# Optimization experiments

Hardware: AMD Instinct MI355X
Metric: run time of the kernel (lower is better)

Reference implementation:

```python
import jax, jax.numpy as jnp
import numpy as np

N = 50000      # nodes
E = 800000     # edges (before self-loops)
F_IN = 768     # num_features
H = 128        # hidden_dim
C = 9          # num_classes
M = 3          # num_mid_layers
BN_EPS = 1e-5

def _glorot(k, shape):
    lim = float(np.sqrt(6.0 / (shape[-2] + shape[-1])))
    return jax.random.uniform(k, shape, jnp.float32, -lim, lim)

def setup_inputs() -> dict:
    key = jax.random.key(0)
    ks = jax.random.split(key, 24)
    x = jax.random.normal(ks[0], (N, F_IN), jnp.float32)
    edge_index = jax.random.randint(ks[1], (2, E), 0, N)
    edge_type = jax.random.randint(ks[2], (E,), 0, 5)
    edge_distance = jax.random.uniform(ks[3], (E,), jnp.float32)
    # GATConv params (heads=1): W [in,out], att_src/att_dst [out], bias [out]
    W0 = _glorot(ks[4], (F_IN, H)); a0s = _glorot(ks[5], (1, H))[0]; a0d = _glorot(ks[6], (1, H))[0]; b0 = jnp.zeros((H,), jnp.float32)
    Wm = _glorot(ks[7], (M, H, H)); ams = _glorot(ks[8], (M, 1, H))[:, 0]; amd = _glorot(ks[9], (M, 1, H))[:, 0]; bm = jnp.zeros((M, H), jnp.float32)
    W4 = _glorot(ks[10], (H, C)); a4s = _glorot(ks[11], (1, C))[0]; a4d = _glorot(ks[12], (1, C))[0]; b4 = jnp.zeros((C,), jnp.float32)
    # BatchNorm params for the M+1 norms actually used in forward (all dim H)
    gamma = jnp.ones((M + 1, H), jnp.float32)
    beta = jnp.zeros((M + 1, H), jnp.float32)
    return {"x": x, "edge_index": edge_index, "edge_type": edge_type, "edge_distance": edge_distance,
            "W0": W0, "a0s": a0s, "a0d": a0d, "b0": b0,
            "Wm": Wm, "ams": ams, "amd": amd, "bm": bm,
            "W4": W4, "a4s": a4s, "a4d": a4d, "b4": b4,
            "gamma": gamma, "beta": beta}

def _leaky(x, s):
    return jnp.where(x >= 0, x, s * x)

def _gat_conv(x, src, dst, W, a_s, a_d, b):
    # x: [N, in] -> h: [N, out]; attention per edge j->i, softmax over incoming edges of i
    h = x @ W
    alpha_src = h @ a_s            # [N]
    alpha_dst = h @ a_d            # [N]
    e = _leaky(alpha_src[src] + alpha_dst[dst], 0.2)   # [Etot]
    m = jax.ops.segment_max(e, dst, num_segments=N)
    ex = jnp.exp(e - m[dst])
    z = jax.ops.segment_sum(ex, dst, num_segments=N)
    alpha = ex / z[dst]
    out = jax.ops.segment_sum(h[src] * alpha[:, None], dst, num_segments=N)
    return out + b

def _bn_train(x, g, be):
    mu = x.mean(0)
    var = x.var(0)   # biased, as BatchNorm1d uses for normalization
    return (x - mu) * jax.lax.rsqrt(var + BN_EPS) * g + be

def reference(x, edge_index, edge_type, edge_distance,
              W0, a0s, a0d, b0, Wm, ams, amd, bm, W4, a4s, a4d, b4, gamma, beta):
    loops = jnp.arange(N, dtype=edge_index.dtype)
    src = jnp.concatenate([edge_index[0], loops])   # add self-loops (PyG default)
    dst = jnp.concatenate([edge_index[1], loops])
    h = _gat_conv(x, src, dst, W0, a0s, a0d, b0)
    for i in range(M):
        t = _leaky(_bn_train(h, gamma[i], beta[i]), 0.1)
        h = _gat_conv(t, src, dst, Wm[i], ams[i], amd[i], bm[i]) + t
    h = _leaky(_bn_train(h, gamma[M], beta[M]), 0.1)
    h = _gat_conv(h, src, dst, W4, a4s, a4d, b4)
    return _leaky(h, 0.1)
```

## Files before the change

### kernel.cpp

```cpp
#include <hip/hip_runtime.h>
#include <hip/hip_bf16.h>

#define N_NODES 50000
#define N_EDGES 800000
#define F_INN   768
#define HID     128
#define N_CLS   9
#define ETOT    (N_EDGES + N_NODES)
#define BN_EPS  1e-5f

typedef __hip_bfloat16 bf16;
typedef __attribute__((ext_vector_type(8))) short bf16x8;
typedef __attribute__((ext_vector_type(4))) float f32x4;

__device__ __forceinline__ float leaky(float v, float s) { return v >= 0.0f ? v : s * v; }
__device__ __forceinline__ int clampn(int s) {
  return ((unsigned)s < (unsigned)N_NODES) ? s : 0;
}
__device__ __forceinline__ short f2bs(float f) {
  bf16 h = __float2bfloat16(f);
  return __builtin_bit_cast(short, h);
}
__device__ __forceinline__ float bs2f(unsigned short u) {
  unsigned v = ((unsigned)u) << 16;
  return __builtin_bit_cast(float, v);
}
__device__ __forceinline__ void gload_lds16(const void* g, void* l) {
  __builtin_amdgcn_global_load_lds((const __attribute__((address_space(1))) void*)g,
                                   (__attribute__((address_space(3))) void*)l, 16, 0, 0);
}

__global__ void k_pack(const float* __restrict__ W0, const float* __restrict__ Wm,
                       short* __restrict__ W0T, short* __restrict__ WmT) {
  int i = blockIdx.x * blockDim.x + threadIdx.x;
  if (i < F_INN * HID) {
    int n = i / F_INN, k = i % F_INN;
    W0T[i] = f2bs(W0[k * HID + n]);
  } else if (i < F_INN * HID + 3 * HID * HID) {
    int j = i - F_INN * HID;
    int l = j / (HID * HID), rem = j % (HID * HID);
    int n = rem / HID, k = rem % HID;
    WmT[j] = f2bs(Wm[(l * HID + k) * HID + n]);
  }
}

__global__ void k_zero(float* p, int n) {
  int i = blockIdx.x * blockDim.x + threadIdx.x;
  if (i < n) p[i] = 0.0f;
}

__global__ void k_init_deg(int* fill) {
  int i = blockIdx.x * blockDim.x + threadIdx.x;
  if (i < N_NODES) fill[i] = 1;
}

__global__ void k_count(const int* __restrict__ dst, int* fill) {
  int e = blockIdx.x * blockDim.x + threadIdx.x;
  if (e < N_EDGES) atomicAdd(&fill[clampn(dst[e])], 1);
}

__global__ void k_scan(int* fill, int* row_ptr) {
  __shared__ int wsum[16], wpre[16];
  int tid = threadIdx.x, lane = tid & 63, wv = tid >> 6;
  int carry = 0;
  for (int base = 0; base < N_NODES; base += 1024) {
    int i = base + tid;
    int v = (i < N_NODES) ? fill[i] : 0;
    if (i < N_NODES) fill[i] = 0;
    int sc = v;
#pragma unroll
    for (int off = 1; off < 64; off <<= 1) {
      int t = __shfl_up(sc, off);
      if (lane >= off) sc += t;
    }
    if (lane == 63) wsum[wv] = sc;
    __syncthreads();
    if (tid < 16) {
      int s = wsum[tid];
#pragma unroll
      for (int off = 1; off < 16; off <<= 1) {
        int t = __shfl_up(s, off);
        if (tid >= off) s += t;
      }
      wpre[tid] = s;
    }
    __syncthreads();
    int woff = wv ? wpre[wv - 1] : 0;
    if (i < N_NODES) row_ptr[i] = carry + woff + sc - v;
    carry += wpre[15];
    __syncthreads();
  }
  if (tid == 0) row_ptr[N_NODES] = carry;
}

__global__ void k_place(const int* __restrict__ src, const int* __restrict__ dst,
                        const int* __restrict__ row_ptr, int* fill, int* csr_src) {
  int id = blockIdx.x * blockDim.x + threadIdx.x;
  if (id >= ETOT) return;
  int s, d;
  if (id < N_EDGES) { s = clampn(src[id]); d = clampn(dst[id]); }
  else { s = id - N_EDGES; d = s; }
  int p = atomicAdd(&fill[d], 1);
  csr_src[row_ptr[d] + p] = s;
}

template <int K, bool BN>
__global__ __launch_bounds__(256, 2)
void k_gemm_mfma(const float* __restrict__ X, const short* __restrict__ BT,
                 const float* __restrict__ scale, const float* __restrict__ shift,
                 const float* __restrict__ a_s, const float* __restrict__ a_d,
                 short* __restrict__ hb, float* __restrict__ asrc,
                 float* __restrict__ adst) {
  constexpr int NP = K / 64;
  constexpr int NB = 4;
  __shared__ short sB[NB][8192];
  int tid = threadIdx.x;
  int w = tid >> 6, lane = tid & 63;
  int m = lane & 15, q = lane >> 4;
  int row0 = blockIdx.x * 64 + w * 16;
  int rowm = row0 + m;
  int rowc = (rowm < N_NODES) ? rowm : 0;
  const float* xbase = X + (size_t)rowc * K + q * 8;
  const short* gb = BT + (size_t)m * K + q * 8;

  f32x4 acc[8];
#pragma unroll
  for (int t = 0; t < 8; ++t) acc[t] = (f32x4){0.f, 0.f, 0.f, 0.f};
  float4 xr[NB][4];

  float scf[K / 32][8], sff[K / 32][8];
  if (BN) {
#pragma unroll
    for (int c = 0; c < K / 32; ++c) {
      int kb = c * 32 + q * 8;
      *(float4*)(&scf[c][0]) = *(const float4*)(scale + kb);
      *(float4*)(&scf[c][4]) = *(const float4*)(scale + kb + 4);
      *(float4*)(&sff[c][0]) = *(const float4*)(shift + kb);
      *(float4*)(&sff[c][4]) = *(const float4*)(shift + kb + 4);
    }
  }

  auto issue = [&](int p) {
    const int buf = p & (NB - 1);
#pragma unroll
    for (int c = 0; c < 4; ++c) {
      int ci = w * 4 + c;
      int t = ci >> 1, kk = ci & 1;
      gload_lds16(gb + (size_t)t * 16 * K + p * 64 + kk * 32, &sB[buf][ci * 512]);
    }
    xr[buf][0] = *(const float4*)(xbase + p * 64);
    xr[buf][1] = *(const float4*)(xbase + p * 64 + 4);
    xr[buf][2] = *(const float4*)(xbase + p * 64 + 32);
    xr[buf][3] = *(const float4*)(xbase + p * 64 + 36);
  };

  issue(0);
  if (NP > 1) issue(1);

#pragma unroll
  for (int p = 0; p < NP; ++p) {
    if (p + 2 < NP) issue(p + 2);
    if (p + 2 < NP)      asm volatile("s_waitcnt vmcnt(16)" ::: "memory");
    else if (p + 1 < NP) asm volatile("s_waitcnt vmcnt(8)" ::: "memory");
    else                 asm volatile("s_waitcnt vmcnt(0)" ::: "memory");
    __builtin_amdgcn_s_barrier();

    const int cur = p & (NB - 1);
    const char* sbb = (const char*)&sB[cur][0] + ((size_t)lane << 4);
#pragma unroll
    for (int kk = 0; kk < 2; ++kk) {
      float xv[8];
      *(float4*)(xv)     = xr[cur][kk * 2];
      *(float4*)(xv + 4) = xr[cur][kk * 2 + 1];
      if (BN) {
#pragma unroll
        for (int j = 0; j < 8; ++j)
          xv[j] = leaky(xv[j] * scf[p * 2 + kk][j] + sff[p * 2 + kk][j], 0.1f);
      }
      bf16x8 a;
#pragma unroll
      for (int j = 0; j < 8; ++j) a[j] = f2bs(xv[j]);
#pragma unroll
      for (int t = 0; t < 8; ++t) {
        bf16x8 b = *(const bf16x8*)(sbb + ((t * 2 + kk) << 10));
        acc[t] = __builtin_amdgcn_mfma_f32_16x16x32_bf16(a, b, acc[t], 0, 0, 0);
      }
    }
  }

  float sr[4] = {0.f, 0.f, 0.f, 0.f}, dr[4] = {0.f, 0.f, 0.f, 0.f};
  int rowq = row0 + q * 4;
#pragma unroll
  for (int t = 0; t < 8; ++t) {
    float av = a_s[t * 16 + m], dv = a_d[t * 16 + m];
#pragma unroll
    for (int r = 0; r < 4; ++r) {
      float c = acc[t][r];
      if (rowq + r < N_NODES)
        hb[(size_t)(rowq + r) * HID + t * 16 + m] = f2bs(c);
      sr[r] += c * av;
      dr[r] += c * dv;
    }
  }
#pragma unroll
  for (int r = 0; r < 4; ++r) {
#pragma unroll
    for (int off = 1; off < 16; off <<= 1) {
      sr[r] += __shfl_xor(sr[r], off);
      dr[r] += __shfl_xor(dr[r], off);
    }
  }
  if (m == 0) {
#pragma unroll
    for (int r = 0; r < 4; ++r) {
      if (rowq + r < N_NODES) {
        asrc[rowq + r] = sr[r];
        adst[rowq + r] = dr[r];
      }
    }
  }
}

__device__ __forceinline__ void acc8(float* a, float e, uint4 v) {
  a[0] += e * bs2f((unsigned short)(v.x & 0xffffu));
  a[1] += e * bs2f((unsigned short)(v.x >> 16));
  a[2] += e * bs2f((unsigned short)(v.y & 0xffffu));
  a[3] += e * bs2f((unsigned short)(v.y >> 16));
  a[4] += e * bs2f((unsigned short)(v.z & 0xffffu));
  a[5] += e * bs2f((unsigned short)(v.z >> 16));
  a[6] += e * bs2f((unsigned short)(v.w & 0xffffu));
  a[7] += e * bs2f((unsigned short)(v.w >> 16));
}

__global__ void k_agg128(const unsigned short* __restrict__ h, const float* __restrict__ asrc,
                         const float* __restrict__ adst, const int* __restrict__ row_ptr,
                         const int* __restrict__ csr_src, const float* __restrict__ bias,
                         const float* __restrict__ hres, const float* __restrict__ scale,
                         const float* __restrict__ shift, float* __restrict__ out) {
  __shared__ int   lds_ss[4][64];
  __shared__ float lds_ex[4][64];
  int wid = (blockIdx.x * blockDim.x + threadIdx.x) >> 6;
  int lane = threadIdx.x & 63;
  int w = (threadIdx.x >> 6) & 3;
  if (wid >= N_NODES) return;
  int beg = row_ptr[wid], end = row_ptr[wid + 1];
  float adsti = adst[wid];
  float mx = -1e30f;
  for (int cb = beg; cb < end; cb += 64) {
    int e = cb + lane;
    if (e < end) {
      int s = clampn(csr_src[e]);
      mx = fmaxf(mx, leaky(asrc[s] + adsti, 0.2f));
    }
  }
#pragma unroll
  for (int off = 1; off < 64; off <<= 1) mx = fmaxf(mx, __shfl_xor(mx, off));
  int g = lane & 15;
  int es = lane >> 4;
  float z = 0.f;
  float a[8];
#pragma unroll
  for (int k = 0; k < 8; ++k) a[k] = 0.f;
  for (int cb = beg; cb < end; cb += 64) {
    int cnt = min(64, end - cb);
    int sl = 0;
    float ex = 0.f;
    if (lane < cnt) {
      sl = clampn(csr_src[cb + lane]);
      ex = __expf(leaky(asrc[sl] + adsti, 0.2f) - mx);
    }
    lds_ss[w][lane] = sl;
    lds_ex[w][lane] = ex;
    __builtin_amdgcn_wave_barrier();
    float zp = ex;
#pragma unroll
    for (int off = 1; off < 64; off <<= 1) zp += __shfl_xor(zp, off);
    z += zp;
    for (int jb = 0; jb < cnt; jb += 8) {
      int j0 = jb + es, j1 = jb + 4 + es;
      int s0 = lds_ss[w][j0]; float e0 = lds_ex[w][j0];
      int s1 = lds_ss[w][j1]; float e1 = lds_ex[w][j1];
      uint4 v0 = *(const uint4*)(h + (size_t)s0 * HID + g * 8);
      uint4 v1 = *(const uint4*)(h + (size_t)s1 * HID + g * 8);
      acc8(a, e0, v0);
      acc8(a, e1, v1);
    }
    __builtin_amdgcn_wave_barrier();
  }
#pragma unroll
  for (int k = 0; k < 8; ++k) {
    a[k] += __shfl_xor(a[k], 16);
    a[k] += __shfl_xor(a[k], 32);
  }
  float inv = (z > 0.0f) ? 1.0f / z : 0.0f;
  if (lane < 16) {
    int c0 = g * 8;
    float hr[8];
    if (scale) {
      *(float4*)(hr)     = *(const float4*)(hres + (size_t)wid * HID + c0);
      *(float4*)(hr + 4) = *(const float4*)(hres + (size_t)wid * HID + c0 + 4);
    }
    float o[8];
#pragma unroll
    for (int k = 0; k < 8; ++k) {
      o[k] = a[k] * inv + bias[c0 + k];
      if (scale) o[k] += leaky(hr[k] * scale[c0 + k] + shift[c0 + k], 0.1f);
    }
    *(float4*)(out + (size_t)wid * HID + c0)     = *(float4*)(o);
    *(float4*)(out + (size_t)wid * HID + c0 + 4) = *(float4*)(o + 4);
  }
}

__global__ void k_bn_stats(const float* __restrict__ h, float* bnsum, float* bnsumsq) {
  int f = threadIdx.x;
  int r0 = blockIdx.x * 128;
  int r1 = min(r0 + 128, N_NODES);
  float s = 0.0f, s2 = 0.0f;
#pragma unroll 8
  for (int r = r0; r < r1; ++r) {
    float v = h[(size_t)r * HID + f];
    s += v;
    s2 += v * v;
  }
  atomicAdd(&bnsum[f], s);
  atomicAdd(&bnsumsq[f], s2);
}

__global__ void k_bn_final(const float* __restrict__ bnsum, const float* __restrict__ bnsumsq,
                           const float* __restrict__ gamma, const float* __restrict__ beta,
                           float* bnscale, float* bnshift) {
  int f = threadIdx.x;
  float mu = bnsum[f] / (float)N_NODES;
  float var = bnsumsq[f] / (float)N_NODES - mu * mu;
  var = fmaxf(var, 0.0f);
  float rstd = rsqrtf(var + BN_EPS);
  float g = gamma[f];
  bnscale[f] = g * rstd;
  bnshift[f] = beta[f] - mu * g * rstd;
}

__global__ void k_final_gemm(const float* __restrict__ h, const float* __restrict__ scale,
                             const float* __restrict__ shift, const float* __restrict__ W4,
                             const float* __restrict__ a4s, const float* __restrict__ a4d,
                             float* __restrict__ h4, float* __restrict__ asrc,
                             float* __restrict__ adst) {
  int row = (blockIdx.x * blockDim.x + threadIdx.x) >> 6;
  int lane = threadIdx.x & 63;
  if (row >= N_NODES) return;
  float t0 = leaky(h[(size_t)row * HID + lane] * scale[lane] + shift[lane], 0.1f);
  float t1 = leaky(h[(size_t)row * HID + 64 + lane] * scale[64 + lane] + shift[64 + lane], 0.1f);
  float myv = 0.0f, s = 0.0f, d = 0.0f;
#pragma unroll
  for (int c = 0; c < N_CLS; ++c) {
    float p = t0 * W4[lane * N_CLS + c] + t1 * W4[(lane + 64) * N_CLS + c];
#pragma unroll
    for (int m = 32; m; m >>= 1) p += __shfl_xor(p, m);
    s += p * a4s[c];
    d += p * a4d[c];
    if (lane == c) myv = p;
  }
  if (lane < N_CLS) h4[(size_t)row * N_CLS + lane] = myv;
  if (lane == 0) { asrc[row] = s; adst[row] = d; }
}

__global__ void k_final_agg(const float* __restrict__ h4, const float* __restrict__ asrc,
                            const float* __restrict__ adst, const int* __restrict__ row_ptr,
                            const int* __restrict__ csr_src, const float* __restrict__ b4,
                            float* __restrict__ out) {
  int wid = (blockIdx.x * blockDim.x + threadIdx.x) >> 6;
  int lane = threadIdx.x & 63;
  if (wid >= N_NODES) return;
  int beg = row_ptr[wid], end = row_ptr[wid + 1];
  float adsti = adst[wid];
  float mx = -1e30f;
  int e = beg;
  for (; e + 4 <= end; e += 4) {
    int s0 = clampn(csr_src[e]),     s1 = clampn(csr_src[e + 1]);
    int s2 = clampn(csr_src[e + 2]), s3 = clampn(csr_src[e + 3]);
    float v0 = leaky(asrc[s0] + adsti, 0.2f);
    float v1 = leaky(asrc[s1] + adsti, 0.2f);
    float v2 = leaky(asrc[s2] + adsti, 0.2f);
    float v3 = leaky(asrc[s3] + adsti, 0.2f);
    mx = fmaxf(mx, fmaxf(fmaxf(v0, v1), fmaxf(v2, v3)));
  }
  for (; e < end; ++e) {
    int s = clampn(csr_src[e]);
    mx = fmaxf(mx, leaky(asrc[s] + adsti, 0.2f));
  }
  float z = 0.0f, a = 0.0f;
  e = beg;
  for (; e + 4 <= end; e += 4) {
    int s0 = clampn(csr_src[e]),     s1 = clampn(csr_src[e + 1]);
    int s2 = clampn(csr_src[e + 2]), s3 = clampn(csr_src[e + 3]);
    float ex0 = __expf(leaky(asrc[s0] + adsti, 0.2f) - mx);
    float ex1 = __expf(leaky(asrc[s1] + adsti, 0.2f) - mx);
    float ex2 = __expf(leaky(asrc[s2] + adsti, 0.2f) - mx);
    float ex3 = __expf(leaky(asrc[s3] + adsti, 0.2f) - mx);
    z += (ex0 + ex1) + (ex2 + ex3);
    if (lane < N_CLS) {
      float h0 = h4[(size_t)s0 * N_CLS + lane];
      float h1 = h4[(size_t)s1 * N_CLS + lane];
      float h2 = h4[(size_t)s2 * N_CLS + lane];
      float h3 = h4[(size_t)s3 * N_CLS + lane];
      a += ex0 * h0 + ex1 * h1 + ex2 * h2 + ex3 * h3;
    }
  }
  for (; e < end; ++e) {
    int s = clampn(csr_src[e]);
    float ex = __expf(leaky(asrc[s] + adsti, 0.2f) - mx);
    z += ex;
    if (lane < N_CLS) a += ex * h4[(size_t)s * N_CLS + lane];
  }
  if (lane < N_CLS) {
    float o = (z > 0.0f) ? a / z : 0.0f;
    o = leaky(o + b4[lane], 0.1f);
    out[(size_t)wid * N_CLS + lane] = o;
  }
}

extern "C" void kernel_launch(void* const* d_in, const int* in_sizes, int n_in,
                              void* d_out, int out_size, void* d_ws, size_t ws_size,
                              hipStream_t stream) {
  const float* x   = (const float*)d_in[0];
  const int*   ei  = (const int*)d_in[1];
  const int*   src = ei;
  const int*   dst = ei + N_EDGES;
  const float* W0  = (const float*)d_in[4];
  const float* a0s = (const float*)d_in[5];
  const float* a0d = (const float*)d_in[6];
  const float* b0  = (const float*)d_in[7];
  const float* Wm  = (const float*)d_in[8];
  const float* ams = (const float*)d_in[9];
  const float* amd = (const float*)d_in[10];
  const float* bm  = (const float*)d_in[11];
  const float* W4  = (const float*)d_in[12];
  const float* a4s = (const float*)d_in[13];
  const float* a4d = (const float*)d_in[14];
  const float* b4  = (const float*)d_in[15];
  const float* gam = (const float*)d_in[16];
  const float* bet = (const float*)d_in[17];
  float* out = (float*)d_out;

  int* row_ptr   = (int*)d_ws;
  int* fill      = row_ptr + 50004;
  int* csr_src   = fill + N_NODES;
  short* W0T     = (short*)(csr_src + ETOT);
  short* WmT     = W0T + F_INN * HID;
  short* bufA    = WmT + 3 * HID * HID;
  float* asrc    = (float*)(bufA + (size_t)N_NODES * HID);
  float* adst    = asrc + N_NODES;
  float* bnsum   = adst + N_NODES;
  float* bnsumsq = bnsum + HID;
  float* bnscale = bnsumsq + HID;
  float* bnshift = bnscale + HID;
  float* h4      = bnshift + HID;
  float* bufB    = h4 + (size_t)N_NODES * N_CLS;

  const int B256 = 256;
  int gN    = (N_NODES + B256 - 1) / B256;
  int gE    = (N_EDGES + B256 - 1) / B256;
  int gET   = (ETOT + B256 - 1) / B256;
  int gWav  = (N_NODES + 3) / 4;
  int gMfma = (N_NODES + 63) / 64;
  int gBN   = (N_NODES + 127) / 128;
  int gPack = (F_INN * HID + 3 * HID * HID + B256 - 1) / B256;

  k_pack<<<gPack, B256, 0, stream>>>(W0, Wm, W0T, WmT);
  k_init_deg<<<gN, B256, 0, stream>>>(fill);
  k_count<<<gE, B256, 0, stream>>>(dst, fill);
  k_scan<<<1, 1024, 0, stream>>>(fill, row_ptr);
  k_place<<<gET, B256, 0, stream>>>(src, dst, row_ptr, fill, csr_src);

  k_gemm_mfma<F_INN, false><<<gMfma, B256, 0, stream>>>(x, W0T, nullptr, nullptr,
                                                        a0s, a0d, bufA, asrc, adst);
  k_agg128<<<gWav, B256, 0, stream>>>((const unsigned short*)bufA, asrc, adst, row_ptr,
                                      csr_src, b0, nullptr, nullptr, nullptr, bufB);

  for (int i = 0; i < 3; ++i) {
    k_zero<<<1, 256, 0, stream>>>(bnsum, 2 * HID);
    k_bn_stats<<<gBN, HID, 0, stream>>>(bufB, bnsum, bnsumsq);
    k_bn_final<<<1, HID, 0, stream>>>(bnsum, bnsumsq, gam + i * HID, bet + i * HID,
                                      bnscale, bnshift);
    k_gemm_mfma<HID, true><<<gMfma, B256, 0, stream>>>(bufB, WmT + i * HID * HID,
                                                       bnscale, bnshift,
                                                       ams + i * HID, amd + i * HID,
                                                       bufA, asrc, adst);
    k_agg128<<<gWav, B256, 0, stream>>>((const unsigned short*)bufA, asrc, adst, row_ptr,
                                        csr_src, bm + i * HID, bufB, bnscale, bnshift, bufB);
  }

  k_zero<<<1, 256, 0, stream>>>(bnsum, 2 * HID);
  k_bn_stats<<<gBN, HID, 0, stream>>>(bufB, bnsum, bnsumsq);
  k_bn_final<<<1, HID, 0, stream>>>(bnsum, bnsumsq, gam + 3 * HID, bet + 3 * HID,
                                    bnscale, bnshift);
  k_final_gemm<<<gWav, B256, 0, stream>>>(bufB, bnscale, bnshift, W4, a4s, a4d,
                                          h4, asrc, adst);
  k_final_agg<<<gWav, B256, 0, stream>>>(h4, asrc, adst, row_ptr, csr_src, b4, out);
}
```

Baseline: 950.9 us.

## Restructure GEMM tiling, fold BN finalize into consumers, add single-pass aggregation

The MFMA GEMM now handles 16 rows per 512-thread block. Each wave computes a 16-column slice, the X tile is staged in LDS with an XOR swizzle, and weights are register double-buffered from global. The separate zero and BN-finalize kernels are removed: consumers recompute scale and shift from the raw sums, and the aggregation kernel zeroes the next stats buffer through ping-pong buffers. Both aggregation kernels gain a single-pass path for nodes with at most 64 incoming edges, and the final aggregation is parallelised across edges within a wave. The risks are redundant per-thread BN math and more global weight traffic per block.

New measurement: 808.0 us. -15.0%, faster.

```diff
diff --git a/kernel.cpp b/kernel.cpp
--- a/kernel.cpp
+++ b/kernel.cpp
@@ -8,6 +8,7 @@
 #define N_CLS   9
 #define ETOT    (N_EDGES + N_NODES)
 #define BN_EPS  1e-5f
+#define INV_N   (1.0f / (float)N_NODES)
 
 typedef __hip_bfloat16 bf16;
 typedef __attribute__((ext_vector_type(8))) short bf16x8;
@@ -44,11 +45,6 @@
   }
 }
 
-__global__ void k_zero(float* p, int n) {
-  int i = blockIdx.x * blockDim.x + threadIdx.x;
-  if (i < n) p[i] = 0.0f;
-}
-
 __global__ void k_init_deg(int* fill) {
   int i = blockIdx.x * blockDim.x + threadIdx.x;
   if (i < N_NODES) fill[i] = 1;
@@ -105,102 +101,101 @@
 }
 
 template <int K, bool BN>
-__global__ __launch_bounds__(256, 2)
+__global__ __launch_bounds__(512, 5)
 void k_gemm_mfma(const float* __restrict__ X, const short* __restrict__ BT,
-                 const float* __restrict__ scale, const float* __restrict__ shift,
+                 const float* __restrict__ stats, const float* __restrict__ gamma,
+                 const float* __restrict__ beta,
                  const float* __restrict__ a_s, const float* __restrict__ a_d,
                  short* __restrict__ hb, float* __restrict__ asrc,
                  float* __restrict__ adst) {
-  constexpr int NP = K / 64;
-  constexpr int NB = 4;
-  __shared__ short sB[NB][8192];
+  constexpr int NS = K / 32;
+  constexpr int SPC = 4;
+  constexpr int CH = NS / SPC;
+  constexpr int ROWB = K * 4;
+  constexpr int XB = 16 * ROWB;
+  __shared__ float4 xs4[XB / 16];
+  __shared__ float psA[8][16], psD[8][16];
+  __shared__ float scs[HID], sfs[HID];
+  char* xs = (char*)xs4;
+
   int tid = threadIdx.x;
-  int w = tid >> 6, lane = tid & 63;
+  int wid = tid >> 6, lane = tid & 63;
   int m = lane & 15, q = lane >> 4;
-  int row0 = blockIdx.x * 64 + w * 16;
-  int rowm = row0 + m;
-  int rowc = (rowm < N_NODES) ? rowm : 0;
-  const float* xbase = X + (size_t)rowc * K + q * 8;
-  const short* gb = BT + (size_t)m * K + q * 8;
-
-  f32x4 acc[8];
-#pragma unroll
-  for (int t = 0; t < 8; ++t) acc[t] = (f32x4){0.f, 0.f, 0.f, 0.f};
-  float4 xr[NB][4];
-
-  float scf[K / 32][8], sff[K / 32][8];
-  if (BN) {
-#pragma unroll
-    for (int c = 0; c < K / 32; ++c) {
-      int kb = c * 32 + q * 8;
-      *(float4*)(&scf[c][0]) = *(const float4*)(scale + kb);
-      *(float4*)(&scf[c][4]) = *(const float4*)(scale + kb + 4);
-      *(float4*)(&sff[c][0]) = *(const float4*)(shift + kb);
-      *(float4*)(&sff[c][4]) = *(const float4*)(shift + kb + 4);
-    }
-  }
-
-  auto issue = [&](int p) {
-    const int buf = p & (NB - 1);
-#pragma unroll
-    for (int c = 0; c < 4; ++c) {
-      int ci = w * 4 + c;
-      int t = ci >> 1, kk = ci & 1;
-      gload_lds16(gb + (size_t)t * 16 * K + p * 64 + kk * 32, &sB[buf][ci * 512]);
-    }
-    xr[buf][0] = *(const float4*)(xbase + p * 64);
-    xr[buf][1] = *(const float4*)(xbase + p * 64 + 4);
-    xr[buf][2] = *(const float4*)(xbase + p * 64 + 32);
-    xr[buf][3] = *(const float4*)(xbase + p * 64 + 36);
+  int row0 = blockIdx.x * 16;
+  int col0 = wid * 16;
+
+  const short* bbase = BT + (size_t)(col0 + m) * K + q * 8;
+  f32x4 acc = (f32x4){0.f, 0.f, 0.f, 0.f};
+  bf16x8 bb0[SPC], bb1[SPC];
+
+  auto loadC = [&](bf16x8* dst, int c) {
+#pragma unroll
+    for (int i = 0; i < SPC; ++i)
+      dst[i] = *(const bf16x8*)(bbase + (size_t)(c * SPC + i) * 32);
   };
-
-  issue(0);
-  if (NP > 1) issue(1);
-
-#pragma unroll
-  for (int p = 0; p < NP; ++p) {
-    if (p + 2 < NP) issue(p + 2);
-    if (p + 2 < NP)      asm volatile("s_waitcnt vmcnt(16)" ::: "memory");
-    else if (p + 1 < NP) asm volatile("s_waitcnt vmcnt(8)" ::: "memory");
-    else                 asm volatile("s_waitcnt vmcnt(0)" ::: "memory");
-    __builtin_amdgcn_s_barrier();
-
-    const int cur = p & (NB - 1);
-    const char* sbb = (const char*)&sB[cur][0] + ((size_t)lane << 4);
-#pragma unroll
-    for (int kk = 0; kk < 2; ++kk) {
-      float xv[8];
-      *(float4*)(xv)     = xr[cur][kk * 2];
-      *(float4*)(xv + 4) = xr[cur][kk * 2 + 1];
+  auto computeC = [&](const bf16x8* bw, int c) {
+#pragma unroll
+    for (int i = 0; i < SPC; ++i) {
+      int s = c * SPC + i;
+      int kb = s * 128 + q * 32;
+      int sw = (m & 7) << 4;
+      float4 x0 = *(const float4*)(xs + m * ROWB + (kb ^ sw));
+      float4 x1 = *(const float4*)(xs + m * ROWB + ((kb + 16) ^ sw));
+      float xv[8] = {x0.x, x0.y, x0.z, x0.w, x1.x, x1.y, x1.z, x1.w};
       if (BN) {
-#pragma unroll
-        for (int j = 0; j < 8; ++j)
-          xv[j] = leaky(xv[j] * scf[p * 2 + kk][j] + sff[p * 2 + kk][j], 0.1f);
+        int k0 = s * 32 + q * 8;
+#pragma unroll
+        for (int j = 0; j < 8; ++j) xv[j] = leaky(xv[j] * scs[k0 + j] + sfs[k0 + j], 0.1f);
       }
       bf16x8 a;
 #pragma unroll
       for (int j = 0; j < 8; ++j) a[j] = f2bs(xv[j]);
-#pragma unroll
-      for (int t = 0; t < 8; ++t) {
-        bf16x8 b = *(const bf16x8*)(sbb + ((t * 2 + kk) << 10));
-        acc[t] = __builtin_amdgcn_mfma_f32_16x16x32_bf16(a, b, acc[t], 0, 0, 0);
-      }
-    }
-  }
-
-  float sr[4] = {0.f, 0.f, 0.f, 0.f}, dr[4] = {0.f, 0.f, 0.f, 0.f};
-  int rowq = row0 + q * 4;
-#pragma unroll
-  for (int t = 0; t < 8; ++t) {
-    float av = a_s[t * 16 + m], dv = a_d[t * 16 + m];
-#pragma unroll
-    for (int r = 0; r < 4; ++r) {
-      float c = acc[t][r];
-      if (rowq + r < N_NODES)
-        hb[(size_t)(rowq + r) * HID + t * 16 + m] = f2bs(c);
-      sr[r] += c * av;
-      dr[r] += c * dv;
-    }
+      acc = __builtin_amdgcn_mfma_f32_16x16x32_bf16(a, bw[i], acc, 0, 0, 0);
+    }
+  };
+
+  if (BN && tid < HID) {
+    float mu = stats[tid] * INV_N;
+    float var = fmaxf(stats[HID + tid] * INV_N - mu * mu, 0.0f);
+    float rs = rsqrtf(var + BN_EPS);
+    float g = gamma[tid];
+    scs[tid] = g * rs;
+    sfs[tid] = beta[tid] - mu * g * rs;
+  }
+
+  loadC(bb0, 0);
+  if (CH > 1) loadC(bb1, 1);
+  asm volatile("" ::: "memory");
+  constexpr int ROUNDS = XB / 8192;
+#pragma unroll
+  for (int r = 0; r < ROUNDS; ++r) {
+    int o = r * 8192 + tid * 16;
+    int row = o / ROWB;
+    int bb = o - row * ROWB;
+    int sw = (row & 7) << 4;
+    gload_lds16((const char*)X + (size_t)(row0 + row) * ROWB + (bb ^ sw), xs + o);
+  }
+  __syncthreads();
+
+#pragma unroll
+  for (int c = 0; c < CH; ++c) {
+    if (c & 1) {
+      computeC(bb1, c);
+      if (c + 2 < CH) { loadC(bb1, c + 2); asm volatile("" ::: "memory"); }
+    } else {
+      computeC(bb0, c);
+      if (c + 2 < CH) { loadC(bb0, c + 2); asm volatile("" ::: "memory"); }
+    }
+  }
+
+  float av = a_s[col0 + m], dv = a_d[col0 + m];
+  float sr[4], dr[4];
+#pragma unroll
+  for (int r = 0; r < 4; ++r) {
+    float cc = acc[r];
+    hb[(size_t)(row0 + q * 4 + r) * HID + col0 + m] = f2bs(cc);
+    sr[r] = cc * av;
+    dr[r] = cc * dv;
   }
 #pragma unroll
   for (int r = 0; r < 4; ++r) {
@@ -213,11 +208,17 @@
   if (m == 0) {
 #pragma unroll
     for (int r = 0; r < 4; ++r) {
-      if (rowq + r < N_NODES) {
-        asrc[rowq + r] = sr[r];
-        adst[rowq + r] = dr[r];
-      }
-    }
+      psA[wid][q * 4 + r] = sr[r];
+      psD[wid][q * 4 + r] = dr[r];
+    }
+  }
+  __syncthreads();
+  if (tid < 16) {
+    float s = 0.f, d = 0.f;
+#pragma unroll
+    for (int w2 = 0; w2 < 8; ++w2) { s += psA[w2][tid]; d += psD[w2][tid]; }
+    asrc[row0 + tid] = s;
+    adst[row0 + tid] = d;
   }
 }
 
@@ -235,83 +236,122 @@
 __global__ void k_agg128(const unsigned short* __restrict__ h, const float* __restrict__ asrc,
                          const float* __restrict__ adst, const int* __restrict__ row_ptr,
                          const int* __restrict__ csr_src, const float* __restrict__ bias,
-                         const float* __restrict__ hres, const float* __restrict__ scale,
-                         const float* __restrict__ shift, float* __restrict__ out) {
+                         const float* __restrict__ hres, const float* __restrict__ stats,
+                         const float* __restrict__ gamma, const float* __restrict__ beta,
+                         float* __restrict__ out, float* __restrict__ zeroP) {
   __shared__ int   lds_ss[4][64];
   __shared__ float lds_ex[4][64];
+  if (zeroP && blockIdx.x == 0 && threadIdx.x < 256) zeroP[threadIdx.x] = 0.0f;
   int wid = (blockIdx.x * blockDim.x + threadIdx.x) >> 6;
   int lane = threadIdx.x & 63;
   int w = (threadIdx.x >> 6) & 3;
   if (wid >= N_NODES) return;
   int beg = row_ptr[wid], end = row_ptr[wid + 1];
+  int cnt0 = end - beg;
   float adsti = adst[wid];
-  float mx = -1e30f;
-  for (int cb = beg; cb < end; cb += 64) {
-    int e = cb + lane;
-    if (e < end) {
-      int s = clampn(csr_src[e]);
-      mx = fmaxf(mx, leaky(asrc[s] + adsti, 0.2f));
-    }
-  }
-#pragma unroll
-  for (int off = 1; off < 64; off <<= 1) mx = fmaxf(mx, __shfl_xor(mx, off));
-  int g = lane & 15;
-  int es = lane >> 4;
+  int g = lane & 15, es = lane >> 4;
   float z = 0.f;
   float a[8];
 #pragma unroll
   for (int k = 0; k < 8; ++k) a[k] = 0.f;
-  for (int cb = beg; cb < end; cb += 64) {
-    int cnt = min(64, end - cb);
+
+  if (cnt0 <= 64) {
     int sl = 0;
-    float ex = 0.f;
-    if (lane < cnt) {
-      sl = clampn(csr_src[cb + lane]);
-      ex = __expf(leaky(asrc[sl] + adsti, 0.2f) - mx);
-    }
+    float v = -1e30f;
+    if (lane < cnt0) {
+      sl = clampn(csr_src[beg + lane]);
+      v = leaky(asrc[sl] + adsti, 0.2f);
+    }
+    float mx = v;
+#pragma unroll
+    for (int off = 1; off < 64; off <<= 1) mx = fmaxf(mx, __shfl_xor(mx, off));
+    float ex = (lane < cnt0) ? __expf(v - mx) : 0.f;
     lds_ss[w][lane] = sl;
     lds_ex[w][lane] = ex;
     __builtin_amdgcn_wave_barrier();
-    float zp = ex;
-#pragma unroll
-    for (int off = 1; off < 64; off <<= 1) zp += __shfl_xor(zp, off);
-    z += zp;
-    for (int jb = 0; jb < cnt; jb += 8) {
+    float zs = 0.f;
+    for (int jb = 0; jb < cnt0; jb += 8) {
       int j0 = jb + es, j1 = jb + 4 + es;
       int s0 = lds_ss[w][j0]; float e0 = lds_ex[w][j0];
       int s1 = lds_ss[w][j1]; float e1 = lds_ex[w][j1];
       uint4 v0 = *(const uint4*)(h + (size_t)s0 * HID + g * 8);
       uint4 v1 = *(const uint4*)(h + (size_t)s1 * HID + g * 8);
+      zs += e0 + e1;
       acc8(a, e0, v0);
       acc8(a, e1, v1);
     }
-    __builtin_amdgcn_wave_barrier();
+    z = zs;
+  } else {
+    float mx = -1e30f;
+    for (int cb = beg; cb < end; cb += 64) {
+      int e = cb + lane;
+      if (e < end) {
+        int s = clampn(csr_src[e]);
+        mx = fmaxf(mx, leaky(asrc[s] + adsti, 0.2f));
+      }
+    }
+#pragma unroll
+    for (int off = 1; off < 64; off <<= 1) mx = fmaxf(mx, __shfl_xor(mx, off));
+    float zs = 0.f;
+    for (int cb = beg; cb < end; cb += 64) {
+      int cnt = min(64, end - cb);
+      int sl = 0;
+      float ex = 0.f;
+      if (lane < cnt) {
+        sl = clampn(csr_src[cb + lane]);
+        ex = __expf(leaky(asrc[sl] + adsti, 0.2f) - mx);
+      }
+      lds_ss[w][lane] = sl;
+      lds_ex[w][lane] = ex;
+      __builtin_amdgcn_wave_barrier();
+      for (int jb = 0; jb < cnt; jb += 8) {
+        int j0 = jb + es, j1 = jb + 4 + es;
+        int s0 = lds_ss[w][j0]; float e0 = lds_ex[w][j0];
+        int s1 = lds_ss[w][j1]; float e1 = lds_ex[w][j1];
+        uint4 v0 = *(const uint4*)(h + (size_t)s0 * HID + g * 8);
+        uint4 v1 = *(const uint4*)(h + (size_t)s1 * HID + g * 8);
+        zs += e0 + e1;
+        acc8(a, e0, v0);
+        acc8(a, e1, v1);
+      }
+      __builtin_amdgcn_wave_barrier();
+    }
+    z = zs;
   }
 #pragma unroll
   for (int k = 0; k < 8; ++k) {
     a[k] += __shfl_xor(a[k], 16);
     a[k] += __shfl_xor(a[k], 32);
   }
+  z += __shfl_xor(z, 16);
+  z += __shfl_xor(z, 32);
   float inv = (z > 0.0f) ? 1.0f / z : 0.0f;
   if (lane < 16) {
     int c0 = g * 8;
-    float hr[8];
-    if (scale) {
+    float o[8];
+#pragma unroll
+    for (int k = 0; k < 8; ++k) o[k] = a[k] * inv + bias[c0 + k];
+    if (hres) {
+      float hr[8];
       *(float4*)(hr)     = *(const float4*)(hres + (size_t)wid * HID + c0);
       *(float4*)(hr + 4) = *(const float4*)(hres + (size_t)wid * HID + c0 + 4);
-    }
-    float o[8];
-#pragma unroll
-    for (int k = 0; k < 8; ++k) {
-      o[k] = a[k] * inv + bias[c0 + k];
-      if (scale) o[k] += leaky(hr[k] * scale[c0 + k] + shift[c0 + k], 0.1f);
+#pragma unroll
+      for (int k = 0; k < 8; ++k) {
+        int c = c0 + k;
+        float mu = stats[c] * INV_N;
+        float var = fmaxf(stats[HID + c] * INV_N - mu * mu, 0.0f);
+        float rs = rsqrtf(var + BN_EPS);
+        float sc = gamma[c] * rs;
+        float sf = beta[c] - mu * sc;
+        o[k] += leaky(hr[k] * sc + sf, 0.1f);
+      }
     }
     *(float4*)(out + (size_t)wid * HID + c0)     = *(float4*)(o);
     *(float4*)(out + (size_t)wid * HID + c0 + 4) = *(float4*)(o + 4);
   }
 }
 
-__global__ void k_bn_stats(const float* __restrict__ h, float* bnsum, float* bnsumsq) {
+__global__ void k_bn_stats(const float* __restrict__ h, float* stats) {
   int f = threadIdx.x;
   int r0 = blockIdx.x * 128;
   int r1 = min(r0 + 128, N_NODES);
@@ -322,33 +362,30 @@
     s += v;
     s2 += v * v;
   }
-  atomicAdd(&bnsum[f], s);
-  atomicAdd(&bnsumsq[f], s2);
-}
-
-__global__ void k_bn_final(const float* __restrict__ bnsum, const float* __restrict__ bnsumsq,
-                           const float* __restrict__ gamma, const float* __restrict__ beta,
-                           float* bnscale, float* bnshift) {
-  int f = threadIdx.x;
-  float mu = bnsum[f] / (float)N_NODES;
-  float var = bnsumsq[f] / (float)N_NODES - mu * mu;
-  var = fmaxf(var, 0.0f);
-  float rstd = rsqrtf(var + BN_EPS);
-  float g = gamma[f];
-  bnscale[f] = g * rstd;
-  bnshift[f] = beta[f] - mu * g * rstd;
-}
-
-__global__ void k_final_gemm(const float* __restrict__ h, const float* __restrict__ scale,
-                             const float* __restrict__ shift, const float* __restrict__ W4,
+  atomicAdd(&stats[f], s);
+  atomicAdd(&stats[HID + f], s2);
+}
+
+__global__ void k_final_gemm(const float* __restrict__ h, const float* __restrict__ stats,
+                             const float* __restrict__ gamma, const float* __restrict__ beta,
+                             const float* __restrict__ W4,
                              const float* __restrict__ a4s, const float* __restrict__ a4d,
                              float* __restrict__ h4, float* __restrict__ asrc,
                              float* __restrict__ adst) {
   int row = (blockIdx.x * blockDim.x + threadIdx.x) >> 6;
   int lane = threadIdx.x & 63;
   if (row >= N_NODES) return;
-  float t0 = leaky(h[(size_t)row * HID + lane] * scale[lane] + shift[lane], 0.1f);
-  float t1 = leaky(h[(size_t)row * HID + 64 + lane] * scale[64 + lane] + shift[64 + lane], 0.1f);
+  int c1 = lane + 64;
+  float mu0 = stats[lane] * INV_N;
+  float va0 = fmaxf(stats[HID + lane] * INV_N - mu0 * mu0, 0.0f);
+  float rs0 = rsqrtf(va0 + BN_EPS);
+  float sc0 = gamma[lane] * rs0, sf0 = beta[lane] - mu0 * sc0;
+  float mu1 = stats[c1] * INV_N;
+  float va1 = fmaxf(stats[HID + c1] * INV_N - mu1 * mu1, 0.0f);
+  float rs1 = rsqrtf(va1 + BN_EPS);
+  float sc1 = gamma[c1] * rs1, sf1 = beta[c1] - mu1 * sc1;
+  float t0 = leaky(h[(size_t)row * HID + lane] * sc0 + sf0, 0.1f);
+  float t1 = leaky(h[(size_t)row * HID + c1] * sc1 + sf1, 0.1f);
   float myv = 0.0f, s = 0.0f, d = 0.0f;
 #pragma unroll
   for (int c = 0; c < N_CLS; ++c) {
@@ -367,52 +404,75 @@
                             const float* __restrict__ adst, const int* __restrict__ row_ptr,
                             const int* __restrict__ csr_src, const float* __restrict__ b4,
                             float* __restrict__ out) {
+  __shared__ int   lds_ss[4][64];
+  __shared__ float lds_ex[4][64];
   int wid = (blockIdx.x * blockDim.x + threadIdx.x) >> 6;
   int lane = threadIdx.x & 63;
+  int w = (threadIdx.x >> 6) & 3;
   if (wid >= N_NODES) return;
   int beg = row_ptr[wid], end = row_ptr[wid + 1];
+  int cnt0 = end - beg;
   float adsti = adst[wid];
-  float mx = -1e30f;
-  int e = beg;
-  for (; e + 4 <= end; e += 4) {
-    int s0 = clampn(csr_src[e]),     s1 = clampn(csr_src[e + 1]);
-    int s2 = clampn(csr_src[e + 2]), s3 = clampn(csr_src[e + 3]);
-    float v0 = leaky(asrc[s0] + adsti, 0.2f);
-    float v1 = leaky(asrc[s1] + adsti, 0.2f);
-    float v2 = leaky(asrc[s2] + adsti, 0.2f);
-    float v3 = leaky(asrc[s3] + adsti, 0.2f);
-    mx = fmaxf(mx, fmaxf(fmaxf(v0, v1), fmaxf(v2, v3)));
-  }
-  for (; e < end; ++e) {
-    int s = clampn(csr_src[e]);
-    mx = fmaxf(mx, leaky(asrc[s] + adsti, 0.2f));
-  }
-  float z = 0.0f, a = 0.0f;
-  e = beg;
-  for (; e + 4 <= end; e += 4) {
-    int s0 = clampn(csr_src[e]),     s1 = clampn(csr_src[e + 1]);
-    int s2 = clampn(csr_src[e + 2]), s3 = clampn(csr_src[e + 3]);
-    float ex0 = __expf(leaky(asrc[s0] + adsti, 0.2f) - mx);
-    float ex1 = __expf(leaky(asrc[s1] + adsti, 0.2f) - mx);
-    float ex2 = __expf(leaky(asrc[s2] + adsti, 0.2f) - mx);
-    float ex3 = __expf(leaky(asrc[s3] + adsti, 0.2f) - mx);
-    z += (ex0 + ex1) + (ex2 + ex3);
-    if (lane < N_CLS) {
-      float h0 = h4[(size_t)s0 * N_CLS + lane];
-      float h1 = h4[(size_t)s1 * N_CLS + lane];
-      float h2 = h4[(size_t)s2 * N_CLS + lane];
-      float h3 = h4[(size_t)s3 * N_CLS + lane];
-      a += ex0 * h0 + ex1 * h1 + ex2 * h2 + ex3 * h3;
-    }
-  }
-  for (; e < end; ++e) {
-    int s = clampn(csr_src[e]);
-    float ex = __expf(leaky(asrc[s] + adsti, 0.2f) - mx);
-    z += ex;
-    if (lane < N_CLS) a += ex * h4[(size_t)s * N_CLS + lane];
-  }
+  int g = lane & 15, es = lane >> 4;
+  float zs = 0.f, av = 0.f;
+  if (cnt0 <= 64) {
+    int sl = 0;
+    float v = -1e30f;
+    if (lane < cnt0) {
+      sl = clampn(csr_src[beg + lane]);
+      v = leaky(asrc[sl] + adsti, 0.2f);
+    }
+    float mx = v;
+#pragma unroll
+    for (int off = 1; off < 64; off <<= 1) mx = fmaxf(mx, __shfl_xor(mx, off));
+    float ex = (lane < cnt0) ? __expf(v - mx) : 0.f;
+    lds_ss[w][lane] = sl;
+    lds_ex[w][lane] = ex;
+    __builtin_amdgcn_wave_barrier();
+    for (int jb = 0; jb < cnt0; jb += 4) {
+      int j = jb + es;
+      int s = lds_ss[w][j];
+      float e = lds_ex[w][j];
+      zs += e;
+      if (g < N_CLS) av += e * h4[(size_t)s * N_CLS + g];
+    }
+  } else {
+    float mx = -1e30f;
+    for (int cb = beg; cb < end; cb += 64) {
+      int e = cb + lane;
+      if (e < end) {
+        int s = clampn(csr_src[e]);
+        mx = fmaxf(mx, leaky(asrc[s] + adsti, 0.2f));
+      }
+    }
+#pragma unroll
+    for (int off = 1; off < 64; off <<= 1) mx = fmaxf(mx, __shfl_xor(mx, off));
+    for (int cb = beg; cb < end; cb += 64) {
+      int cnt = min(64, end - cb);
+      int sl = 0;
+      float ex = 0.f;
+      if (lane < cnt) {
+        sl = clampn(csr_src[cb + lane]);
+        ex = __expf(leaky(asrc[sl] + adsti, 0.2f) - mx);
+      }
+      lds_ss[w][lane] = sl;
+      lds_ex[w][lane] = ex;
+      __builtin_amdgcn_wave_barrier();
+      for (int jb = 0; jb < cnt; jb += 4) {
+        int j = jb + es;
+        int s = lds_ss[w][j];
+        float e = lds_ex[w][j];
+        zs += e;
+        if (g < N_CLS) av += e * h4[(size_t)s * N_CLS + g];
+      }
+      __builtin_amdgcn_wave_barrier();
+    }
+  }
+  float z = zs;
+  z += __shfl_xor(z, 16); z += __shfl_xor(z, 32);
+  av += __shfl_xor(av, 16); av += __shfl_xor(av, 32);
   if (lane < N_CLS) {
-    float o = (z > 0.0f) ? a / z : 0.0f;
+    float o = (z > 0.0f) ? av / z : 0.0f;
     o = leaky(o + b4[lane], 0.1f);
     out[(size_t)wid * N_CLS + lane] = o;
   }
@@ -449,19 +509,17 @@
   short* bufA    = WmT + 3 * HID * HID;
   float* asrc    = (float*)(bufA + (size_t)N_NODES * HID);
   float* adst    = asrc + N_NODES;
-  float* bnsum   = adst + N_NODES;
-  float* bnsumsq = bnsum + HID;
-  float* bnscale = bnsumsq + HID;
-  float* bnshift = bnscale + HID;
-  float* h4      = bnshift + HID;
+  float* pstat   = adst + N_NODES;
+  float* h4      = pstat + 512;
   float* bufB    = h4 + (size_t)N_NODES * N_CLS;
+  float* PST[2]  = {pstat, pstat + 256};
 
   const int B256 = 256;
   int gN    = (N_NODES + B256 - 1) / B256;
   int gE    = (N_EDGES + B256 - 1) / B256;
   int gET   = (ETOT + B256 - 1) / B256;
   int gWav  = (N_NODES + 3) / 4;
-  int gMfma = (N_NODES + 63) / 64;
+  int gMfma = N_NODES / 16;
   int gBN   = (N_NODES + 127) / 128;
   int gPack = (F_INN * HID + 3 * HID * HID + B256 - 1) / B256;
 
@@ -471,29 +529,25 @@
   k_scan<<<1, 1024, 0, stream>>>(fill, row_ptr);
   k_place<<<gET, B256, 0, stream>>>(src, dst, row_ptr, fill, csr_src);
 
-  k_gemm_mfma<F_INN, false><<<gMfma, B256, 0, stream>>>(x, W0T, nullptr, nullptr,
-                                                        a0s, a0d, bufA, asrc, adst);
+  k_gemm_mfma<F_INN, false><<<gMfma, 512, 0, stream>>>(x, W0T, nullptr, nullptr, nullptr,
+                                                       a0s, a0d, bufA, asrc, adst);
   k_agg128<<<gWav, B256, 0, stream>>>((const unsigned short*)bufA, asrc, adst, row_ptr,
-                                      csr_src, b0, nullptr, nullptr, nullptr, bufB);
+                                      csr_src, b0, nullptr, nullptr, nullptr, nullptr,
+                                      bufB, PST[0]);
 
   for (int i = 0; i < 3; ++i) {
-    k_zero<<<1, 256, 0, stream>>>(bnsum, 2 * HID);
-    k_bn_stats<<<gBN, HID, 0, stream>>>(bufB, bnsum, bnsumsq);
-    k_bn_final<<<1, HID, 0, stream>>>(bnsum, bnsumsq, gam + i * HID, bet + i * HID,
-                                      bnscale, bnshift);
-    k_gemm_mfma<HID, true><<<gMfma, B256, 0, stream>>>(bufB, WmT + i * HID * HID,
-                                                       bnscale, bnshift,
-                                                       ams + i * HID, amd + i * HID,
-                                                       bufA, asrc, adst);
+    k_bn_stats<<<gBN, HID, 0, stream>>>(bufB, PST[i & 1]);
+    k_gemm_mfma<HID, true><<<gMfma, 512, 0, stream>>>(bufB, WmT + i * HID * HID,
+                                                      PST[i & 1], gam + i * HID, bet + i * HID,
+                                                      ams + i * HID, amd + i * HID,
+                                                      bufA, asrc, adst);
     k_agg128<<<gWav, B256, 0, stream>>>((const unsigned short*)bufA, asrc, adst, row_ptr,
-                                        csr_src, bm + i * HID, bufB, bnscale, bnshift, bufB);
-  }
-
-  k_zero<<<1, 256, 0, stream>>>(bnsum, 2 * HID);
-  k_bn_stats<<<gBN, HID, 0, stream>>>(bufB, bnsum, bnsumsq);
-  k_bn_final<<<1, HID, 0, stream>>>(bnsum, bnsumsq, gam + 3 * HID, bet + 3 * HID,
-                                    bnscale, bnshift);
-  k_final_gemm<<<gWav, B256, 0, stream>>>(bufB, bnscale, bnshift, W4, a4s, a4d,
-                                          h4, asrc, adst);
+                                        csr_src, bm + i * HID, bufB, PST[i & 1],
+                                        gam + i * HID, bet + i * HID, bufB, PST[(i + 1) & 1]);
+  }
+
+  k_bn_stats<<<gBN, HID, 0, stream>>>(bufB, PST[1]);
+  k_final_gemm<<<gWav, B256, 0, stream>>>(bufB, PST[1], gam + 3 * HID, bet + 3 * HID,
+                                          W4, a4s, a4d, h4, asrc, adst);
   k_final_agg<<<gWav, B256, 0, stream>>>(h4, asrc, adst, row_ptr, csr_src, b4, out);
 }
```
